# Performance work log

Measured on AMD Instinct MI355X. Metric: run time of the kernel, lower is better.

The kernel has to match this reference:

```python
import jax, jax.numpy as jnp
import numpy as np

B = 1024      # batch
DIN = 103     # generator/encoder input dim
L1, L2 = 64, 32   # encoder layer widths (latent = 32)
E = 8         # NUM_EXPERTS
GH = 64       # gating hidden width
H = 256       # generator hidden width
DOUT = 51     # generator output dim
EPS = 1e-5    # BatchNorm eps


def setup_inputs() -> dict:
    key = jax.random.key(0)
    ks = jax.random.split(key, 24)
    s = 0.05
    f32 = jnp.float32
    return {
        "x": jax.random.normal(ks[0], (B, DIN), f32),
        # encoder Linear + BN params
        "w1": jax.random.normal(ks[1], (L1, DIN), f32) * s,
        "b1": jnp.zeros((L1,), f32),
        "gamma1": jnp.ones((L1,), f32),
        "beta1": jnp.zeros((L1,), f32),
        "w2": jax.random.normal(ks[2], (L2, L1), f32) * s,
        "b2": jnp.zeros((L2,), f32),
        "gamma2": jnp.ones((L2,), f32),
        "beta2": jnp.zeros((L2,), f32),
        # gating MLP (latent 32 -> GH -> GH -> E, ELU, softmax)
        "gw1": jax.random.normal(ks[3], (GH, L2), f32) * s,
        "gb1": jnp.zeros((GH,), f32),
        "gw2": jax.random.normal(ks[4], (GH, GH), f32) * s,
        "gb2": jnp.zeros((GH,), f32),
        "gw3": jax.random.normal(ks[5], (E, GH), f32) * s,
        "gb3": jnp.zeros((E,), f32),
        # expert weight banks for 3-layer generator (MANN style)
        "ew1": jax.random.normal(ks[6], (E, DIN, H), f32) * s,
        "eb1": jnp.zeros((E, H), f32),
        "ew2": jax.random.normal(ks[7], (E, H, H), f32) * s,
        "eb2": jnp.zeros((E, H), f32),
        "ew3": jax.random.normal(ks[8], (E, H, DOUT), f32) * s,
        "eb3": jnp.zeros((E, DOUT), f32),
    }


def _batchnorm(h, gamma, beta):
    # training-mode BatchNorm1d: per-batch mean/var (biased var, matching torch)
    m = jnp.mean(h, axis=0)
    v = jnp.mean((h - m) ** 2, axis=0)
    return gamma * (h - m) * jax.lax.rsqrt(v + EPS) + beta


def reference(x, w1, b1, gamma1, beta1, w2, b2, gamma2, beta2,
              gw1, gb1, gw2, gb2, gw3, gb3,
              ew1, eb1, ew2, eb2, ew3, eb3):
    # in-place scale of last 3 features (x[:,100:103] *= 100)
    xs = x.at[:, 100:103].multiply(100.0)
    # encoder: Linear -> BN -> ReLU, twice
    h = jax.nn.relu(_batchnorm(xs @ w1.T + b1, gamma1, beta1))
    latent = jax.nn.relu(_batchnorm(h @ w2.T + b2, gamma2, beta2))
    # gating network -> blending coefficients BC [B, E]
    g = jax.nn.elu(latent @ gw1.T + gb1)
    g = jax.nn.elu(g @ gw2.T + gb2)
    bc = jax.nn.softmax(g @ gw3.T + gb3, axis=-1)
    # MANN-style generator: per-sample expert-blended weights
    wb1 = jnp.einsum('be,eih->bih', bc, ew1)   # [B, DIN, H]
    h1 = jax.nn.elu(jnp.einsum('bi,bih->bh', xs, wb1) + bc @ eb1)
    wb2 = jnp.einsum('be,ehk->bhk', bc, ew2)   # [B, H, H]
    h2 = jax.nn.elu(jnp.einsum('bh,bhk->bk', h1, wb2) + bc @ eb2)
    wb3 = jnp.einsum('be,eho->bho', bc, ew3)   # [B, H, DOUT]
    out = jnp.einsum('bh,bho->bo', h2, wb3) + bc @ eb3
    return out
```

## Files before the change

### kernel.cpp

```cpp
#include <hip/hip_runtime.h>
#include <math.h>


#define DIN 103
#define NE  8
#define HH  256
#define DOUT 51
#define EPSBN 1e-5f

typedef __attribute__((ext_vector_type(8))) short bf16x8;
typedef __attribute__((ext_vector_type(4))) float f32x4;
typedef __attribute__((ext_vector_type(8))) unsigned short us8;
typedef unsigned short ushort_t;

__device__ __forceinline__ float eluf(float v) { return v > 0.f ? v : (expf(v) - 1.f); }
__device__ __forceinline__ unsigned short bf16h(float f) {
  unsigned u = __float_as_uint(f);
  u += 0x7FFFu + ((u >> 16) & 1u);
  return (unsigned short)(u >> 16);
}
__device__ __forceinline__ float bf16f(unsigned short h) { return __uint_as_float(((unsigned)h) << 16); }
__device__ __forceinline__ void split_bf16(float v, unsigned short& h, unsigned short& l) {
  h = bf16h(v);
  l = bf16h(v - bf16f(h));
}
#define MFMA __builtin_amdgcn_mfma_f32_16x16x32_bf16

#define O_SLOTS1 0
#define O_SLOTS2 8192
#define O_H1RAW  20480
#define O_H2RAW  86016
#define O_XSH    118784
#define O_XSL    184320
#define O_E1H    258048
#define O_E1L    389120
#define O_E2H    520192
#define O_E3H    782336

__global__ __launch_bounds__(256) void k_prep_enc1(
    const float* __restrict__ x, const float* __restrict__ w1, const float* __restrict__ b1,
    const float* __restrict__ ew1, const float* __restrict__ ew2, const float* __restrict__ ew3,
    float* __restrict__ ws) {
  __shared__ union {
    float tile[32][65];
    float xt[16][104];
    struct { float w1L[64 * DIN]; float xr[16][104]; float hb[16][64]; } e1;
  } sm;
  int bk = blockIdx.x, t = threadIdx.x;
  int l2 = t & 63, c = l2 & 15, q = l2 >> 4;

  if (bk < 256) {
    int nh = bk & 3, kc = (bk >> 2) & 7, e = bk >> 5;
    int k0 = kc * 32, n0 = nh * 64;
#pragma unroll
    for (int i = 0; i < 8; ++i) {
      int kl = (t >> 6) + i * 4;
      sm.tile[kl][t & 63] = ew2[((size_t)e * HH + k0 + kl) * HH + n0 + (t & 63)];
    }
    __syncthreads();
    int nsl = t >> 6;
    us8 H8;
#pragma unroll
    for (int j = 0; j < 8; ++j) H8[j] = bf16h(sm.tile[q * 8 + j][nsl * 16 + c]);
    size_t dst = (((size_t)(e * 16 + nh * 4 + nsl)) * 8 + kc) * 512 + l2 * 8;
    *(us8*)((ushort_t*)(ws + O_E2H) + dst) = H8;
  } else if (bk < 384) {
    int b2 = bk - 256;
    int nh = b2 & 3, kc = (b2 >> 2) & 3, e = b2 >> 4;
    int k0 = kc * 32, n0 = nh * 64;
#pragma unroll
    for (int i = 0; i < 8; ++i) {
      int kl = (t >> 6) + i * 4;
      int k = k0 + kl;
      sm.tile[kl][t & 63] = (k < DIN) ? ew1[((size_t)e * DIN + k) * HH + n0 + (t & 63)] : 0.f;
    }
    __syncthreads();
    int nsl = t >> 6;
    us8 H8, L8;
#pragma unroll
    for (int j = 0; j < 8; ++j) {
      unsigned short h, lo; split_bf16(sm.tile[q * 8 + j][nsl * 16 + c], h, lo);
      H8[j] = h; L8[j] = lo;
    }
    size_t dst = (((size_t)(e * 16 + nh * 4 + nsl)) * 4 + kc) * 512 + l2 * 8;
    *(us8*)((ushort_t*)(ws + O_E1H) + dst) = H8;
    *(us8*)((ushort_t*)(ws + O_E1L) + dst) = L8;
  } else if (bk < 448) {
    int b2 = bk - 384;
    int kc = b2 & 7, e = b2 >> 3;
    int k0 = kc * 32;
#pragma unroll
    for (int i = 0; i < 8; ++i) {
      int kl = (t >> 6) + i * 4;
      int n = t & 63;
      sm.tile[kl][n] = (n < DOUT) ? ew3[((size_t)e * HH + k0 + kl) * DOUT + n] : 0.f;
    }
    __syncthreads();
    int nsl = t >> 6;
    us8 H8;
#pragma unroll
    for (int j = 0; j < 8; ++j) H8[j] = bf16h(sm.tile[q * 8 + j][nsl * 16 + c]);
    size_t dst = (((size_t)(e * 4 + nsl)) * 8 + kc) * 512 + l2 * 8;
    *(us8*)((ushort_t*)(ws + O_E3H) + dst) = H8;
  } else if (bk < 512) {
    int msub = bk - 448;
    for (int i = t; i < 16 * 104; i += 256) {
      int b = i / 104, k = i - b * 104;
      float v = 0.f;
      if (k < DIN) { v = x[(size_t)(msub * 16 + b) * DIN + k]; if (k >= 100) v *= 100.f; }
      sm.xt[b][k] = v;
    }
    __syncthreads();
    int kc = t >> 6;
    int m = c;
    us8 H8, L8;
#pragma unroll
    for (int j = 0; j < 8; ++j) {
      int k = kc * 32 + q * 8 + j;
      float v = (k < 104) ? sm.xt[m][k] : 0.f;
      unsigned short h, lo; split_bf16(v, h, lo);
      H8[j] = h; L8[j] = lo;
    }
    size_t dst = ((size_t)msub * 4 + kc) * 512 + l2 * 8;
    *(us8*)((ushort_t*)(ws + O_XSH) + dst) = H8;
    *(us8*)((ushort_t*)(ws + O_XSL) + dst) = L8;
  } else {
    float* slots1 = ws + O_SLOTS1;
    float* h1raw  = ws + O_H1RAW;
    int bkl = bk - 512;
    int r0 = bkl * 16;
    for (int i = t; i < 64 * DIN; i += 256) sm.e1.w1L[i] = w1[i];
    for (int i = t; i < 16 * 104; i += 256) {
      int r = i / 104, c2 = i - r * 104;
      float v = 0.f;
      if (c2 < DIN) { v = x[(size_t)(r0 + r) * DIN + c2]; if (c2 >= 100) v *= 100.f; }
      sm.e1.xr[r][c2] = v;
    }
    __syncthreads();
#pragma unroll
    for (int i = 0; i < 4; ++i) {
      int idx = t + i * 256;
      int r = idx >> 6, j = idx & 63;
      float acc = b1[j];
      for (int k = 0; k < DIN; ++k) acc = fmaf(sm.e1.xr[r][k], sm.e1.w1L[j * DIN + k], acc);
      sm.e1.hb[r][j] = acc;
      h1raw[(size_t)(r0 + r) * 64 + j] = acc;
    }
    __syncthreads();
    if (t < 64) {
      float s = 0.f, qq = 0.f;
      for (int r = 0; r < 16; ++r) { float v = sm.e1.hb[r][t]; s += v; qq += v * v; }
      slots1[bkl * 128 + t] = s;
      slots1[bkl * 128 + 64 + t] = qq;
    }
  }
}

__global__ __launch_bounds__(256) void k_enc2(
    const float* __restrict__ gamma1, const float* __restrict__ beta1,
    const float* __restrict__ w2, const float* __restrict__ b2, float* __restrict__ ws) {
  __shared__ float w2T[64 * 33];
  __shared__ float red[128];
  __shared__ float sc1[64], sh1[64];
  __shared__ float h1b[16][64];
  __shared__ float hb2[16][32];
  float* slots1 = ws + O_SLOTS1;
  float* slots2 = ws + O_SLOTS2;
  float* h1raw  = ws + O_H1RAW;
  float* h2raw  = ws + O_H2RAW;
  int bk = blockIdx.x, t = threadIdx.x;
  int R0 = bk * 16;
  for (int i = t; i < 2048; i += 256) { int j = i >> 6, k = i & 63; w2T[k * 33 + j] = w2[i]; }
  if (t < 128) {
    float s = 0.f;
    for (int b = 0; b < 64; ++b) s += slots1[b * 128 + t];
    red[t] = s;
  }
  __syncthreads();
  if (t < 64) {
    float m = red[t] * (1.f / 1024.f);
    float v = red[64 + t] * (1.f / 1024.f) - m * m;
    float sc = gamma1[t] * rsqrtf(v + EPSBN);
    sc1[t] = sc; sh1[t] = beta1[t] - m * sc;
  }
  __syncthreads();
#pragma unroll
  for (int i = 0; i < 4; ++i) {
    int idx = t + i * 256;
    int r = idx >> 6, k = idx & 63;
    h1b[r][k] = fmaxf(fmaf(h1raw[(size_t)(R0 + r) * 64 + k], sc1[k], sh1[k]), 0.f);
  }
  __syncthreads();
#pragma unroll
  for (int i = 0; i < 2; ++i) {
    int o = t + i * 256;
    int r = o >> 5, j = o & 31;
    float acc = b2[j];
    for (int k = 0; k < 64; ++k) acc = fmaf(h1b[r][k], w2T[k * 33 + j], acc);
    hb2[r][j] = acc;
    h2raw[(size_t)(R0 + r) * 32 + j] = acc;
  }
  __syncthreads();
  if (t < 32) {
    float s = 0.f, q = 0.f;
    for (int r = 0; r < 16; ++r) { float v = hb2[r][t]; s += v; q += v * v; }
    slots2[bk * 64 + t] = s;
    slots2[bk * 64 + 32 + t] = q;
  }
}

__global__ __launch_bounds__(512) void k_mega(
    const float* __restrict__ gamma2, const float* __restrict__ beta2,
    const float* __restrict__ gw1, const float* __restrict__ gb1,
    const float* __restrict__ gw2, const float* __restrict__ gb2,
    const float* __restrict__ gw3, const float* __restrict__ gb3,
    const float* __restrict__ eb1, const float* __restrict__ eb2,
    const float* __restrict__ eb3,
    const float* __restrict__ ws, float* __restrict__ out) {
  __shared__ union {
    struct {
      float gw1L[64 * 33];
      float gw2L[64 * 65];
      float gw3L[8 * 65];
      float gb1L[64], gb2L[64], gb3L[8];
      float red2[64], sc2[32], sh2[32];
      float lat[16][32];
      float g1[16][64], g2[16][64];
    } gate;
    struct {
      float hT[256][17];
      float eb[2048];
    } comb;
    struct {
      float p3s[8][16][64];
      float eb3L[8][64];
    } g3;
  } U;
  __shared__ us8 aHv[512], aLv[512];
  __shared__ float bcL[16][8];

  const int bk = blockIdx.x, t = threadIdx.x;
  const int wv = t >> 6, l = t & 63, c = l & 15, quad = l >> 4;
  const int R0 = bk * 16;
  const float* slots2 = ws + O_SLOTS2;
  const float* h2raw  = ws + O_H2RAW;
  const ushort_t* XsH = (const ushort_t*)(ws + O_XSH);
  const ushort_t* XsL = (const ushort_t*)(ws + O_XSL);
  const ushort_t* E1H = (const ushort_t*)(ws + O_E1H);
  const ushort_t* E1L = (const ushort_t*)(ws + O_E1L);
  const ushort_t* E2H = (const ushort_t*)(ws + O_E2H);
  const ushort_t* E3H = (const ushort_t*)(ws + O_E3H);

  for (int i = t; i < 2048; i += 512) { int j = i >> 5, k = i & 31; U.gate.gw1L[j * 33 + k] = gw1[i]; }
  for (int i = t; i < 4096; i += 512) { int j = i >> 6, k = i & 63; U.gate.gw2L[j * 65 + k] = gw2[i]; }
  { int j = t >> 6, k = t & 63; U.gate.gw3L[j * 65 + k] = gw3[t]; }
  if (t < 64) { U.gate.gb1L[t] = gb1[t]; U.gate.gb2L[t] = gb2[t]; }
  if (t < 8) U.gate.gb3L[t] = gb3[t];
  if (t < 64) {
    float s = 0.f;
    for (int b = 0; b < 64; ++b) s += slots2[b * 64 + t];
    U.gate.red2[t] = s;
  }
  __syncthreads();
  if (t < 32) {
    float m = U.gate.red2[t] * (1.f / 1024.f);
    float v = U.gate.red2[32 + t] * (1.f / 1024.f) - m * m;
    float sc = gamma2[t] * rsqrtf(v + EPSBN);
    U.gate.sc2[t] = sc; U.gate.sh2[t] = beta2[t] - m * sc;
  }
  __syncthreads();
  { int r = t >> 5, cc = t & 31;
    U.gate.lat[r][cc] = fmaxf(fmaf(h2raw[(size_t)(R0 + r) * 32 + cc], U.gate.sc2[cc], U.gate.sh2[cc]), 0.f); }
  __syncthreads();
#pragma unroll
  for (int rr = 0; rr < 2; ++rr) {
    int r = wv * 2 + rr;
    float a1 = U.gate.gb1L[l];
    for (int k = 0; k < 32; ++k) a1 = fmaf(U.gate.gw1L[l * 33 + k], U.gate.lat[r][k], a1);
    U.gate.g1[r][l] = eluf(a1);
  }
  __syncthreads();
#pragma unroll
  for (int rr = 0; rr < 2; ++rr) {
    int r = wv * 2 + rr;
    float a2 = U.gate.gb2L[l];
    for (int k = 0; k < 64; ++k) a2 = fmaf(U.gate.gw2L[l * 65 + k], U.gate.g1[r][k], a2);
    U.gate.g2[r][l] = eluf(a2);
  }
  __syncthreads();
#pragma unroll
  for (int rr = 0; rr < 2; ++rr) {
    int r = wv * 2 + rr;
    if (l < 8) {
      float a3 = U.gate.gb3L[l];
      for (int k = 0; k < 64; ++k) a3 = fmaf(U.gate.gw3L[l * 65 + k], U.gate.g2[r][k], a3);
      float mx = a3;
      mx = fmaxf(mx, __shfl_xor(mx, 1));
      mx = fmaxf(mx, __shfl_xor(mx, 2));
      mx = fmaxf(mx, __shfl_xor(mx, 4));
      float p = expf(a3 - mx);
      float sp = p;
      sp += __shfl_xor(sp, 1); sp += __shfl_xor(sp, 2); sp += __shfl_xor(sp, 4);
      bcL[r][l] = p / sp;
    }
  }
  __syncthreads();

  for (int i = t; i < 2048; i += 512) U.comb.eb[i] = eb1[i];
  bf16x8 a1h[4], a1l[4];
#pragma unroll
  for (int kc = 0; kc < 4; ++kc) {
    a1h[kc] = *(const bf16x8*)(XsH + ((size_t)bk * 4 + kc) * 512 + l * 8);
    a1l[kc] = *(const bf16x8*)(XsL + ((size_t)bk * 4 + kc) * 512 + l * 8);
  }
  __syncthreads();
  {
    f32x4 blend[2] = {};
#pragma unroll
    for (int e = 0; e < NE; ++e) {
      float bcv[4];
#pragma unroll
      for (int r = 0; r < 4; ++r) bcv[r] = bcL[quad * 4 + r][e];
#pragma unroll
      for (int nsi = 0; nsi < 2; ++nsi) {
        int ns = wv * 2 + nsi;
        f32x4 acc = {};
#pragma unroll
        for (int kc = 0; kc < 4; ++kc) {
          size_t bo = (((size_t)(e * 16 + ns)) * 4 + kc) * 512 + l * 8;
          bf16x8 bh = *(const bf16x8*)(E1H + bo);
          bf16x8 bl = *(const bf16x8*)(E1L + bo);
          acc = MFMA(a1h[kc], bh, acc, 0, 0, 0);
          acc = MFMA(a1l[kc], bh, acc, 0, 0, 0);
          acc = MFMA(a1h[kc], bl, acc, 0, 0, 0);
        }
        float ebv = U.comb.eb[e * HH + ns * 16 + c];
#pragma unroll
        for (int r = 0; r < 4; ++r) blend[nsi][r] = fmaf(bcv[r], acc[r] + ebv, blend[nsi][r]);
      }
    }
#pragma unroll
    for (int nsi = 0; nsi < 2; ++nsi) {
      int col = (wv * 2 + nsi) * 16 + c;
#pragma unroll
      for (int r = 0; r < 4; ++r) U.comb.hT[col][quad * 4 + r] = eluf(blend[nsi][r]);
    }
  }
  __syncthreads();
  {
    int l2 = t & 63, row = l2 & 15, k0 = (t >> 6) * 32 + (l2 >> 4) * 8;
    us8 H, L;
#pragma unroll
    for (int j = 0; j < 8; ++j) {
      unsigned short h, lo; split_bf16(U.comb.hT[k0 + j][row], h, lo);
      H[j] = h; L[j] = lo;
    }
    aHv[t] = H; aLv[t] = L;
  }
  __syncthreads();

  for (int i = t; i < 2048; i += 512) U.comb.eb[i] = eb2[i];
  bf16x8 a2h[8], a2l[8];
#pragma unroll
  for (int kc = 0; kc < 8; ++kc) {
    a2h[kc] = *(const bf16x8*)&aHv[kc * 64 + l];
    a2l[kc] = *(const bf16x8*)&aLv[kc * 64 + l];
  }
  __syncthreads();
  {
    f32x4 blend[2] = {};
#pragma unroll
    for (int e = 0; e < NE; ++e) {
      float bcv[4];
#pragma unroll
      for (int r = 0; r < 4; ++r) bcv[r] = bcL[quad * 4 + r][e];
#pragma unroll
      for (int nsi = 0; nsi < 2; ++nsi) {
        int ns = wv * 2 + nsi;
        f32x4 acc = {};
#pragma unroll
        for (int kc = 0; kc < 8; ++kc) {
          size_t bo = (((size_t)(e * 16 + ns)) * 8 + kc) * 512 + l * 8;
          bf16x8 bh = *(const bf16x8*)(E2H + bo);
          acc = MFMA(a2h[kc], bh, acc, 0, 0, 0);
          acc = MFMA(a2l[kc], bh, acc, 0, 0, 0);
        }
        float ebv = U.comb.eb[e * HH + ns * 16 + c];
#pragma unroll
        for (int r = 0; r < 4; ++r) blend[nsi][r] = fmaf(bcv[r], acc[r] + ebv, blend[nsi][r]);
      }
    }
#pragma unroll
    for (int nsi = 0; nsi < 2; ++nsi) {
      int col = (wv * 2 + nsi) * 16 + c;
#pragma unroll
      for (int r = 0; r < 4; ++r) U.comb.hT[col][quad * 4 + r] = eluf(blend[nsi][r]);
    }
  }
  __syncthreads();
  {
    int l2 = t & 63, row = l2 & 15, k0 = (t >> 6) * 32 + (l2 >> 4) * 8;
    us8 H, L;
#pragma unroll
    for (int j = 0; j < 8; ++j) {
      unsigned short h, lo; split_bf16(U.comb.hT[k0 + j][row], h, lo);
      H[j] = h; L[j] = lo;
    }
    aHv[t] = H; aLv[t] = L;
  }
  __syncthreads();

  { int e = t >> 6, n = t & 63; U.g3.eb3L[e][n] = (n < DOUT) ? eb3[e * DOUT + n] : 0.f; }
  {
    const int e = wv;
    f32x4 acc[4] = {};
#pragma unroll
    for (int kc = 0; kc < 8; ++kc) {
      bf16x8 ah = *(const bf16x8*)&aHv[kc * 64 + l];
      bf16x8 al = *(const bf16x8*)&aLv[kc * 64 + l];
#pragma unroll
      for (int nsi = 0; nsi < 4; ++nsi) {
        size_t bo = (((size_t)(e * 4 + nsi)) * 8 + kc) * 512 + l * 8;
        bf16x8 bh = *(const bf16x8*)(E3H + bo);
        acc[nsi] = MFMA(ah, bh, acc[nsi], 0, 0, 0);
        acc[nsi] = MFMA(al, bh, acc[nsi], 0, 0, 0);
      }
    }
#pragma unroll
    for (int nsi = 0; nsi < 4; ++nsi)
#pragma unroll
      for (int r = 0; r < 4; ++r)
        U.g3.p3s[e][quad * 4 + r][nsi * 16 + c] = acc[nsi][r];
  }
  __syncthreads();
#pragma unroll
  for (int i = 0; i < 2; ++i) {
    int idx = t + i * 512;
    int row = idx >> 6, col = idx & 63;
    float s = 0.f;
#pragma unroll
    for (int e2 = 0; e2 < 8; ++e2)
      s = fmaf(bcL[row][e2], U.g3.p3s[e2][row][col] + U.g3.eb3L[e2][col], s);
    if (col < DOUT) out[(size_t)(R0 + row) * DOUT + col] = s;
  }
}

extern "C" void kernel_launch(void* const* d_in, const int* in_sizes, int n_in,
                              void* d_out, int out_size, void* d_ws, size_t ws_size,
                              hipStream_t stream) {
  const float* x      = (const float*)d_in[0];
  const float* w1     = (const float*)d_in[1];
  const float* b1     = (const float*)d_in[2];
  const float* gamma1 = (const float*)d_in[3];
  const float* beta1  = (const float*)d_in[4];
  const float* w2     = (const float*)d_in[5];
  const float* b2     = (const float*)d_in[6];
  const float* gamma2 = (const float*)d_in[7];
  const float* beta2  = (const float*)d_in[8];
  const float* gw1    = (const float*)d_in[9];
  const float* gb1    = (const float*)d_in[10];
  const float* gw2    = (const float*)d_in[11];
  const float* gb2    = (const float*)d_in[12];
  const float* gw3    = (const float*)d_in[13];
  const float* gb3    = (const float*)d_in[14];
  const float* ew1    = (const float*)d_in[15];
  const float* eb1    = (const float*)d_in[16];
  const float* ew2    = (const float*)d_in[17];
  const float* eb2    = (const float*)d_in[18];
  const float* ew3    = (const float*)d_in[19];
  const float* eb3    = (const float*)d_in[20];
  float* wsf  = (float*)d_ws;
  float* outp = (float*)d_out;

  k_prep_enc1<<<576, 256, 0, stream>>>(x, w1, b1, ew1, ew2, ew3, wsf);
  k_enc2<<<64, 256, 0, stream>>>(gamma1, beta1, w2, b2, wsf);
  k_mega<<<64, 512, 0, stream>>>(gamma2, beta2, gw1, gb1, gw2, gb2, gw3, gb3,
                                 eb1, eb2, eb3, wsf, outp);
}
```

Before: 156.7 us.

## Split fused generator kernel into three launches with 4x more blocks for layers 1-2

The single 64-block mega kernel is split into three kernels. The layer-1 and layer-2 expert-blend GEMMs now run across 256 blocks, each handling a 64-column slice. Gating coefficients and bf16 hi/lo split activations are passed between kernels through workspace buffers. This raises parallelism on a GPU with many CUs, at the cost of two extra launches, global round-trips for the intermediates, and gating work repeated in each of the four column-group blocks.

```diff
diff --git a/kernel.cpp b/kernel.cpp
--- a/kernel.cpp
+++ b/kernel.cpp
@@ -28,6 +28,7 @@
 
 #define O_SLOTS1 0
 #define O_SLOTS2 8192
+#define O_BCG    12288
 #define O_H1RAW  20480
 #define O_H2RAW  86016
 #define O_XSH    118784
@@ -36,6 +37,10 @@
 #define O_E1L    389120
 #define O_E2H    520192
 #define O_E3H    782336
+#define O_A1H    847872
+#define O_A1L    978944
+#define O_A2H    1110016
+#define O_A2L    1241088
 
 __global__ __launch_bounds__(256) void k_prep_enc1(
     const float* __restrict__ x, const float* __restrict__ w1, const float* __restrict__ b1,
@@ -209,14 +214,12 @@
   }
 }
 
-__global__ __launch_bounds__(512) void k_mega(
+__global__ __launch_bounds__(256) void k_gen1(
     const float* __restrict__ gamma2, const float* __restrict__ beta2,
     const float* __restrict__ gw1, const float* __restrict__ gb1,
     const float* __restrict__ gw2, const float* __restrict__ gb2,
     const float* __restrict__ gw3, const float* __restrict__ gb3,
-    const float* __restrict__ eb1, const float* __restrict__ eb2,
-    const float* __restrict__ eb3,
-    const float* __restrict__ ws, float* __restrict__ out) {
+    const float* __restrict__ eb1, float* __restrict__ ws) {
   __shared__ union {
     struct {
       float gw1L[64 * 33];
@@ -228,32 +231,34 @@
       float g1[16][64], g2[16][64];
     } gate;
     struct {
-      float hT[256][17];
-      float eb[2048];
+      float hT[64][17];
+      float ebs[512];
     } comb;
-    struct {
-      float p3s[8][16][64];
-      float eb3L[8][64];
-    } g3;
   } U;
-  __shared__ us8 aHv[512], aLv[512];
   __shared__ float bcL[16][8];
 
-  const int bk = blockIdx.x, t = threadIdx.x;
+  const int blk = blockIdx.x, t = threadIdx.x;
+  const int m = blk >> 2, g = blk & 3;
   const int wv = t >> 6, l = t & 63, c = l & 15, quad = l >> 4;
-  const int R0 = bk * 16;
+  const int R0 = m * 16;
   const float* slots2 = ws + O_SLOTS2;
   const float* h2raw  = ws + O_H2RAW;
+  float* bcg = ws + O_BCG;
   const ushort_t* XsH = (const ushort_t*)(ws + O_XSH);
   const ushort_t* XsL = (const ushort_t*)(ws + O_XSL);
   const ushort_t* E1H = (const ushort_t*)(ws + O_E1H);
   const ushort_t* E1L = (const ushort_t*)(ws + O_E1L);
-  const ushort_t* E2H = (const ushort_t*)(ws + O_E2H);
-  const ushort_t* E3H = (const ushort_t*)(ws + O_E3H);
-
-  for (int i = t; i < 2048; i += 512) { int j = i >> 5, k = i & 31; U.gate.gw1L[j * 33 + k] = gw1[i]; }
-  for (int i = t; i < 4096; i += 512) { int j = i >> 6, k = i & 63; U.gate.gw2L[j * 65 + k] = gw2[i]; }
-  { int j = t >> 6, k = t & 63; U.gate.gw3L[j * 65 + k] = gw3[t]; }
+
+  bf16x8 a1h[4], a1l[4];
+#pragma unroll
+  for (int kc = 0; kc < 4; ++kc) {
+    a1h[kc] = *(const bf16x8*)(XsH + ((size_t)m * 4 + kc) * 512 + l * 8);
+    a1l[kc] = *(const bf16x8*)(XsL + ((size_t)m * 4 + kc) * 512 + l * 8);
+  }
+
+  for (int i = t; i < 2048; i += 256) { int j = i >> 5, k = i & 31; U.gate.gw1L[j * 33 + k] = gw1[i]; }
+  for (int i = t; i < 4096; i += 256) { int j = i >> 6, k = i & 63; U.gate.gw2L[j * 65 + k] = gw2[i]; }
+  for (int i = t; i < 512; i += 256) { int j = i >> 6, k = i & 63; U.gate.gw3L[j * 65 + k] = gw3[i]; }
   if (t < 64) { U.gate.gb1L[t] = gb1[t]; U.gate.gb2L[t] = gb2[t]; }
   if (t < 8) U.gate.gb3L[t] = gb3[t];
   if (t < 64) {
@@ -263,34 +268,38 @@
   }
   __syncthreads();
   if (t < 32) {
-    float m = U.gate.red2[t] * (1.f / 1024.f);
-    float v = U.gate.red2[32 + t] * (1.f / 1024.f) - m * m;
+    float mm = U.gate.red2[t] * (1.f / 1024.f);
+    float v = U.gate.red2[32 + t] * (1.f / 1024.f) - mm * mm;
     float sc = gamma2[t] * rsqrtf(v + EPSBN);
-    U.gate.sc2[t] = sc; U.gate.sh2[t] = beta2[t] - m * sc;
-  }
-  __syncthreads();
-  { int r = t >> 5, cc = t & 31;
-    U.gate.lat[r][cc] = fmaxf(fmaf(h2raw[(size_t)(R0 + r) * 32 + cc], U.gate.sc2[cc], U.gate.sh2[cc]), 0.f); }
-  __syncthreads();
-#pragma unroll
-  for (int rr = 0; rr < 2; ++rr) {
-    int r = wv * 2 + rr;
+    U.gate.sc2[t] = sc; U.gate.sh2[t] = beta2[t] - mm * sc;
+  }
+  __syncthreads();
+#pragma unroll
+  for (int i = 0; i < 2; ++i) {
+    int idx = t + i * 256;
+    int r = idx >> 5, cc = idx & 31;
+    U.gate.lat[r][cc] = fmaxf(fmaf(h2raw[(size_t)(R0 + r) * 32 + cc], U.gate.sc2[cc], U.gate.sh2[cc]), 0.f);
+  }
+  __syncthreads();
+#pragma unroll
+  for (int rr = 0; rr < 4; ++rr) {
+    int r = wv * 4 + rr;
     float a1 = U.gate.gb1L[l];
     for (int k = 0; k < 32; ++k) a1 = fmaf(U.gate.gw1L[l * 33 + k], U.gate.lat[r][k], a1);
     U.gate.g1[r][l] = eluf(a1);
   }
   __syncthreads();
 #pragma unroll
-  for (int rr = 0; rr < 2; ++rr) {
-    int r = wv * 2 + rr;
+  for (int rr = 0; rr < 4; ++rr) {
+    int r = wv * 4 + rr;
     float a2 = U.gate.gb2L[l];
     for (int k = 0; k < 64; ++k) a2 = fmaf(U.gate.gw2L[l * 65 + k], U.gate.g1[r][k], a2);
     U.gate.g2[r][l] = eluf(a2);
   }
   __syncthreads();
 #pragma unroll
-  for (int rr = 0; rr < 2; ++rr) {
-    int r = wv * 2 + rr;
+  for (int rr = 0; rr < 4; ++rr) {
+    int r = wv * 4 + rr;
     if (l < 8) {
       float a3 = U.gate.gb3L[l];
       for (int k = 0; k < 64; ++k) a3 = fmaf(U.gate.gw3L[l * 65 + k], U.gate.g2[r][k], a3);
@@ -301,137 +310,146 @@
       float p = expf(a3 - mx);
       float sp = p;
       sp += __shfl_xor(sp, 1); sp += __shfl_xor(sp, 2); sp += __shfl_xor(sp, 4);
-      bcL[r][l] = p / sp;
-    }
-  }
-  __syncthreads();
-
-  for (int i = t; i < 2048; i += 512) U.comb.eb[i] = eb1[i];
-  bf16x8 a1h[4], a1l[4];
-#pragma unroll
-  for (int kc = 0; kc < 4; ++kc) {
-    a1h[kc] = *(const bf16x8*)(XsH + ((size_t)bk * 4 + kc) * 512 + l * 8);
-    a1l[kc] = *(const bf16x8*)(XsL + ((size_t)bk * 4 + kc) * 512 + l * 8);
-  }
-  __syncthreads();
-  {
-    f32x4 blend[2] = {};
-#pragma unroll
-    for (int e = 0; e < NE; ++e) {
-      float bcv[4];
-#pragma unroll
-      for (int r = 0; r < 4; ++r) bcv[r] = bcL[quad * 4 + r][e];
-#pragma unroll
-      for (int nsi = 0; nsi < 2; ++nsi) {
-        int ns = wv * 2 + nsi;
-        f32x4 acc = {};
-#pragma unroll
-        for (int kc = 0; kc < 4; ++kc) {
-          size_t bo = (((size_t)(e * 16 + ns)) * 4 + kc) * 512 + l * 8;
-          bf16x8 bh = *(const bf16x8*)(E1H + bo);
-          bf16x8 bl = *(const bf16x8*)(E1L + bo);
-          acc = MFMA(a1h[kc], bh, acc, 0, 0, 0);
-          acc = MFMA(a1l[kc], bh, acc, 0, 0, 0);
-          acc = MFMA(a1h[kc], bl, acc, 0, 0, 0);
-        }
-        float ebv = U.comb.eb[e * HH + ns * 16 + c];
-#pragma unroll
-        for (int r = 0; r < 4; ++r) blend[nsi][r] = fmaf(bcv[r], acc[r] + ebv, blend[nsi][r]);
-      }
-    }
-#pragma unroll
-    for (int nsi = 0; nsi < 2; ++nsi) {
-      int col = (wv * 2 + nsi) * 16 + c;
-#pragma unroll
-      for (int r = 0; r < 4; ++r) U.comb.hT[col][quad * 4 + r] = eluf(blend[nsi][r]);
-    }
-  }
-  __syncthreads();
-  {
-    int l2 = t & 63, row = l2 & 15, k0 = (t >> 6) * 32 + (l2 >> 4) * 8;
+      float bcv = p / sp;
+      bcL[r][l] = bcv;
+      if (g == 0) bcg[(size_t)(R0 + r) * 8 + l] = bcv;
+    }
+  }
+  __syncthreads();
+
+  for (int i = t; i < 512; i += 256) U.comb.ebs[i] = eb1[(i >> 6) * HH + g * 64 + (i & 63)];
+  __syncthreads();
+  const int ns = g * 4 + wv;
+  f32x4 blend = {};
+#pragma unroll
+  for (int e = 0; e < NE; ++e) {
+    float bcv[4];
+#pragma unroll
+    for (int r = 0; r < 4; ++r) bcv[r] = bcL[quad * 4 + r][e];
+    f32x4 acc = {};
+#pragma unroll
+    for (int kc = 0; kc < 4; ++kc) {
+      size_t bo = (((size_t)(e * 16 + ns)) * 4 + kc) * 512 + l * 8;
+      bf16x8 bh = *(const bf16x8*)(E1H + bo);
+      bf16x8 bl = *(const bf16x8*)(E1L + bo);
+      acc = MFMA(a1h[kc], bh, acc, 0, 0, 0);
+      acc = MFMA(a1l[kc], bh, acc, 0, 0, 0);
+      acc = MFMA(a1h[kc], bl, acc, 0, 0, 0);
+    }
+    float ebv = U.comb.ebs[e * 64 + wv * 16 + c];
+#pragma unroll
+    for (int r = 0; r < 4; ++r) blend[r] = fmaf(bcv[r], acc[r] + ebv, blend[r]);
+  }
+#pragma unroll
+  for (int r = 0; r < 4; ++r) U.comb.hT[wv * 16 + c][quad * 4 + r] = eluf(blend[r]);
+  __syncthreads();
+  if (t < 128) {
+    int kcl = t >> 6, l2 = t & 63, row = l2 & 15, k0l = kcl * 32 + (l2 >> 4) * 8;
     us8 H, L;
 #pragma unroll
     for (int j = 0; j < 8; ++j) {
-      unsigned short h, lo; split_bf16(U.comb.hT[k0 + j][row], h, lo);
+      unsigned short h, lo; split_bf16(U.comb.hT[k0l + j][row], h, lo);
       H[j] = h; L[j] = lo;
     }
-    aHv[t] = H; aLv[t] = L;
-  }
-  __syncthreads();
-
-  for (int i = t; i < 2048; i += 512) U.comb.eb[i] = eb2[i];
-  bf16x8 a2h[8], a2l[8];
+    size_t dst = ((size_t)m * 8 + g * 2 + kcl) * 512 + l2 * 8;
+    *(us8*)((ushort_t*)(ws + O_A1H) + dst) = H;
+    *(us8*)((ushort_t*)(ws + O_A1L) + dst) = L;
+  }
+}
+
+__global__ __launch_bounds__(256) void k_gen2n(
+    const float* __restrict__ eb2, float* __restrict__ ws) {
+  __shared__ float hT[64][17];
+  __shared__ float ebs[512];
+  __shared__ float bcL[16][8];
+  const int blk = blockIdx.x, t = threadIdx.x;
+  const int m = blk >> 2, g = blk & 3;
+  const int wv = t >> 6, l = t & 63, c = l & 15, quad = l >> 4;
+  const int R0 = m * 16;
+  const float* bcg = ws + O_BCG;
+  const ushort_t* A1H = (const ushort_t*)(ws + O_A1H);
+  const ushort_t* A1L = (const ushort_t*)(ws + O_A1L);
+  const ushort_t* E2H = (const ushort_t*)(ws + O_E2H);
+
+  if (t < 128) bcL[t >> 3][t & 7] = bcg[(size_t)(R0 + (t >> 3)) * 8 + (t & 7)];
+  for (int i = t; i < 512; i += 256) ebs[i] = eb2[(i >> 6) * HH + g * 64 + (i & 63)];
+  bf16x8 ah[8], al[8];
 #pragma unroll
   for (int kc = 0; kc < 8; ++kc) {
-    a2h[kc] = *(const bf16x8*)&aHv[kc * 64 + l];
-    a2l[kc] = *(const bf16x8*)&aLv[kc * 64 + l];
-  }
-  __syncthreads();
-  {
-    f32x4 blend[2] = {};
-#pragma unroll
-    for (int e = 0; e < NE; ++e) {
-      float bcv[4];
-#pragma unroll
-      for (int r = 0; r < 4; ++r) bcv[r] = bcL[quad * 4 + r][e];
-#pragma unroll
-      for (int nsi = 0; nsi < 2; ++nsi) {
-        int ns = wv * 2 + nsi;
-        f32x4 acc = {};
-#pragma unroll
-        for (int kc = 0; kc < 8; ++kc) {
-          size_t bo = (((size_t)(e * 16 + ns)) * 8 + kc) * 512 + l * 8;
-          bf16x8 bh = *(const bf16x8*)(E2H + bo);
-          acc = MFMA(a2h[kc], bh, acc, 0, 0, 0);
-          acc = MFMA(a2l[kc], bh, acc, 0, 0, 0);
-        }
-        float ebv = U.comb.eb[e * HH + ns * 16 + c];
-#pragma unroll
-        for (int r = 0; r < 4; ++r) blend[nsi][r] = fmaf(bcv[r], acc[r] + ebv, blend[nsi][r]);
-      }
-    }
-#pragma unroll
-    for (int nsi = 0; nsi < 2; ++nsi) {
-      int col = (wv * 2 + nsi) * 16 + c;
-#pragma unroll
-      for (int r = 0; r < 4; ++r) U.comb.hT[col][quad * 4 + r] = eluf(blend[nsi][r]);
-    }
-  }
-  __syncthreads();
-  {
-    int l2 = t & 63, row = l2 & 15, k0 = (t >> 6) * 32 + (l2 >> 4) * 8;
+    ah[kc] = *(const bf16x8*)(A1H + ((size_t)m * 8 + kc) * 512 + l * 8);
+    al[kc] = *(const bf16x8*)(A1L + ((size_t)m * 8 + kc) * 512 + l * 8);
+  }
+  __syncthreads();
+  const int ns = g * 4 + wv;
+  f32x4 blend = {};
+#pragma unroll
+  for (int e = 0; e < NE; ++e) {
+    float bcv[4];
+#pragma unroll
+    for (int r = 0; r < 4; ++r) bcv[r] = bcL[quad * 4 + r][e];
+    f32x4 acc = {};
+#pragma unroll
+    for (int kc = 0; kc < 8; ++kc) {
+      size_t bo = (((size_t)(e * 16 + ns)) * 8 + kc) * 512 + l * 8;
+      bf16x8 bh = *(const bf16x8*)(E2H + bo);
+      acc = MFMA(ah[kc], bh, acc, 0, 0, 0);
+      acc = MFMA(al[kc], bh, acc, 0, 0, 0);
+    }
+    float ebv = ebs[e * 64 + wv * 16 + c];
+#pragma unroll
+    for (int r = 0; r < 4; ++r) blend[r] = fmaf(bcv[r], acc[r] + ebv, blend[r]);
+  }
+#pragma unroll
+  for (int r = 0; r < 4; ++r) hT[wv * 16 + c][quad * 4 + r] = eluf(blend[r]);
+  __syncthreads();
+  if (t < 128) {
+    int kcl = t >> 6, l2 = t & 63, row = l2 & 15, k0l = kcl * 32 + (l2 >> 4) * 8;
     us8 H, L;
 #pragma unroll
     for (int j = 0; j < 8; ++j) {
-      unsigned short h, lo; split_bf16(U.comb.hT[k0 + j][row], h, lo);
+      unsigned short h, lo; split_bf16(hT[k0l + j][row], h, lo);
       H[j] = h; L[j] = lo;
     }
-    aHv[t] = H; aLv[t] = L;
-  }
-  __syncthreads();
-
-  { int e = t >> 6, n = t & 63; U.g3.eb3L[e][n] = (n < DOUT) ? eb3[e * DOUT + n] : 0.f; }
-  {
-    const int e = wv;
-    f32x4 acc[4] = {};
-#pragma unroll
-    for (int kc = 0; kc < 8; ++kc) {
-      bf16x8 ah = *(const bf16x8*)&aHv[kc * 64 + l];
-      bf16x8 al = *(const bf16x8*)&aLv[kc * 64 + l];
-#pragma unroll
-      for (int nsi = 0; nsi < 4; ++nsi) {
-        size_t bo = (((size_t)(e * 4 + nsi)) * 8 + kc) * 512 + l * 8;
-        bf16x8 bh = *(const bf16x8*)(E3H + bo);
-        acc[nsi] = MFMA(ah, bh, acc[nsi], 0, 0, 0);
-        acc[nsi] = MFMA(al, bh, acc[nsi], 0, 0, 0);
-      }
-    }
-#pragma unroll
-    for (int nsi = 0; nsi < 4; ++nsi)
-#pragma unroll
-      for (int r = 0; r < 4; ++r)
-        U.g3.p3s[e][quad * 4 + r][nsi * 16 + c] = acc[nsi][r];
-  }
+    size_t dst = ((size_t)m * 8 + g * 2 + kcl) * 512 + l2 * 8;
+    *(us8*)((ushort_t*)(ws + O_A2H) + dst) = H;
+    *(us8*)((ushort_t*)(ws + O_A2L) + dst) = L;
+  }
+}
+
+__global__ __launch_bounds__(512) void k_gen3(const float* __restrict__ eb3,
+    const float* __restrict__ ws, float* __restrict__ out) {
+  __shared__ float p3s[8][16][64];
+  __shared__ float bcL[16][8];
+  __shared__ float eb3L[8][64];
+  const int bk = blockIdx.x, t = threadIdx.x;
+  const int wv = t >> 6, l = t & 63, c = l & 15, quad = l >> 4;
+  const int R0 = bk * 16;
+  const float* bcg = ws + O_BCG;
+  const ushort_t* A2H = (const ushort_t*)(ws + O_A2H);
+  const ushort_t* A2L = (const ushort_t*)(ws + O_A2L);
+  const ushort_t* E3H = (const ushort_t*)(ws + O_E3H);
+
+  if (t < 128) bcL[t >> 3][t & 7] = bcg[(size_t)(R0 + (t >> 3)) * 8 + (t & 7)];
+  { int e = t >> 6, n = t & 63; eb3L[e][n] = (n < DOUT) ? eb3[e * DOUT + n] : 0.f; }
+  const int e = wv;
+  f32x4 acc[4] = {};
+#pragma unroll
+  for (int kc = 0; kc < 8; ++kc) {
+    bf16x8 ah = *(const bf16x8*)(A2H + ((size_t)bk * 8 + kc) * 512 + l * 8);
+    bf16x8 al = *(const bf16x8*)(A2L + ((size_t)bk * 8 + kc) * 512 + l * 8);
+#pragma unroll
+    for (int nsi = 0; nsi < 4; ++nsi) {
+      size_t bo = (((size_t)(e * 4 + nsi)) * 8 + kc) * 512 + l * 8;
+      bf16x8 bh = *(const bf16x8*)(E3H + bo);
+      acc[nsi] = MFMA(ah, bh, acc[nsi], 0, 0, 0);
+      acc[nsi] = MFMA(al, bh, acc[nsi], 0, 0, 0);
+    }
+  }
+#pragma unroll
+  for (int nsi = 0; nsi < 4; ++nsi)
+#pragma unroll
+    for (int r = 0; r < 4; ++r)
+      p3s[e][quad * 4 + r][nsi * 16 + c] = acc[nsi][r];
   __syncthreads();
 #pragma unroll
   for (int i = 0; i < 2; ++i) {
@@ -440,7 +458,7 @@
     float s = 0.f;
 #pragma unroll
     for (int e2 = 0; e2 < 8; ++e2)
-      s = fmaf(bcL[row][e2], U.g3.p3s[e2][row][col] + U.g3.eb3L[e2][col], s);
+      s = fmaf(bcL[row][e2], p3s[e2][row][col] + eb3L[e2][col], s);
     if (col < DOUT) out[(size_t)(R0 + row) * DOUT + col] = s;
   }
 }
@@ -474,6 +492,7 @@
 
   k_prep_enc1<<<576, 256, 0, stream>>>(x, w1, b1, ew1, ew2, ew3, wsf);
   k_enc2<<<64, 256, 0, stream>>>(gamma1, beta1, w2, b2, wsf);
-  k_mega<<<64, 512, 0, stream>>>(gamma2, beta2, gw1, gb1, gw2, gb2, gw3, gb3,
-                                 eb1, eb2, eb3, wsf, outp);
-}
+  k_gen1<<<256, 256, 0, stream>>>(gamma2, beta2, gw1, gb1, gw2, gb2, gw3, gb3, eb1, wsf);
+  k_gen2n<<<256, 256, 0, stream>>>(eb2, wsf);
+  k_gen3<<<64, 512, 0, stream>>>(eb3, wsf, outp);
+}
```

After: 160.9 us. +2.6%, slower.
